# Kernel optimization log

Measured on AMD Instinct MI355X. Metric: run time of the kernel, lower is better.

The kernel has to match this reference:

```python
import jax, jax.numpy as jnp
import numpy as np

B, N, D, H = 4, 2048, 512, 8
KD = D // H  # per-head key/value dim = 64
NORM = 1.0 / np.sqrt(KD).astype(np.float32)


def setup_inputs() -> dict:
    key = jax.random.key(0)
    kq, km, k1, k2, k3 = jax.random.split(key, 5)
    s = 1.0 / np.sqrt(D)
    return {
        "queries": jax.random.normal(kq, (B, N, D), dtype=jnp.float32),
        "mask": jax.random.randint(km, (B, N, N), 0, 2).astype(jnp.bool_),
        "Wq": jax.random.normal(k1, (D, D), dtype=jnp.float32) * s,
        "Wk": jax.random.normal(k2, (D, D), dtype=jnp.float32) * s,
        "Wc": jax.random.normal(k3, (D, D), dtype=jnp.float32) * s,
    }


def reference(queries, mask, Wq, Wk, Wc):
    # Self-attention path (keys=None, values=None): V uses key_embed (Wk).
    Q = (queries @ Wq.T).reshape(B, N, H, KD)  # [B,N,H,kd]
    K = (queries @ Wk.T).reshape(B, N, H, KD)
    V = K  # original code: V = key_embed(queries) when values is None
    scores = NORM * jnp.einsum("bqhd,bkhd->bhqk", Q, K)  # [B,H,N,N]
    scores = jnp.where(mask[:, None, :, :], -jnp.inf, scores)
    attn = jax.nn.softmax(scores, axis=-1)
    out = jnp.einsum("bhqk,bkhd->bqhd", attn, V).reshape(B, N, H * KD)
    return out @ Wc.T  # [B,N,D]
```

## Files before the change

kernel.cpp:

```cpp
#include <hip/hip_runtime.h>
#include <hip/hip_bf16.h>
#include <math.h>

#define B_ 4
#define N_ 2048
#define D_ 512
#define H_ 8
#define NORM2_ 0.18033688011112042f

typedef __attribute__((ext_vector_type(8))) short short8;
typedef __attribute__((ext_vector_type(4))) float f32x4;
#define MFMA16(a, b, c) __builtin_amdgcn_mfma_f32_16x16x32_bf16(a, b, c, 0, 0, 0)
#define EXP2(x) __builtin_amdgcn_exp2f(x)

static __device__ __forceinline__ uint32_t pk2(float lo, float hi) {
  __hip_bfloat162 h = __float22bfloat162_rn(make_float2(lo, hi));
  return *(reinterpret_cast<uint32_t*>(&h));
}

static __device__ __forceinline__ void async16(const ushort* lds, const ushort* g) {
  __builtin_amdgcn_global_load_lds(
      (const __attribute__((address_space(1))) uint32_t*)g,
      (__attribute__((address_space(3))) uint32_t*)(ushort*)lds, 16, 0, 0);
}

__global__ __launch_bounds__(256) void prep(const float* __restrict__ q,
                                            const int* __restrict__ mask,
                                            const float* __restrict__ wq,
                                            const float* __restrict__ wk,
                                            const float* __restrict__ wc,
                                            ushort* __restrict__ Xb,
                                            ushort* __restrict__ Wb,
                                            uint32_t* __restrict__ pk) {
  const int bx = blockIdx.x;
  if (bx < 2048) {
    const int lane = threadIdx.x & 63;
    const int wid = ((bx << 8) + threadIdx.x) >> 6;
    for (int i = wid; i < 65536; i += 8192) {
      const int4 m = ((const int4*)mask)[(size_t)i * 64 + lane];
      uint32_t nib = (uint32_t)(m.x != 0) | ((uint32_t)(m.y != 0) << 1) |
                     ((uint32_t)(m.z != 0) << 2) | ((uint32_t)(m.w != 0) << 3);
      nib |= __shfl_xor(nib, 1) << 4;
      nib |= __shfl_xor(nib, 2) << 8;
      nib |= __shfl_xor(nib, 4) << 16;
      if ((lane & 7) == 0) pk[i * 8 + (lane >> 3)] = nib;
    }
  } else if (bx < 3072) {
    const int i = ((bx - 2048) << 8) + threadIdx.x;
    for (int j = i; j < 1048576; j += 262144) {
      const float4 v = ((const float4*)q)[j];
      uint2 o; o.x = pk2(v.x, v.y); o.y = pk2(v.z, v.w);
      ((uint2*)Xb)[j] = o;
    }
  } else {
    const int i = ((bx - 3072) << 8) + threadIdx.x;
    for (int j = i; j < 196608; j += 24576) {
      const int wi = j >> 16, off = j & 65535;
      const float* src = (wi == 0) ? wq : (wi == 1) ? wk : wc;
      const float4 v = ((const float4*)src)[off];
      uint2 o; o.x = pk2(v.x, v.y); o.y = pk2(v.z, v.w);
      ((uint2*)Wb)[j] = o;
    }
  }
}

template <int F32OUT>
__global__ __launch_bounds__(256) void gemm128(const ushort* __restrict__ X,
                                               const ushort* __restrict__ W0,
                                               const ushort* __restrict__ W1,
                                               void* __restrict__ C0,
                                               void* __restrict__ C1,
                                               float s0, float s1) {
  const ushort* Wp = (blockIdx.z == 0) ? W0 : W1;
  void* Cp = (blockIdx.z == 0) ? C0 : C1;
  const float sc = (blockIdx.z == 0) ? s0 : s1;
  const int t = threadIdx.x;
  const int w = t >> 6, lane = t & 63, quad = lane >> 4, c = lane & 15;
  const int wm = w & 1, wn = w >> 1;
  const int n0 = blockIdx.x * 128, m0 = blockIdx.y * 128;
  __shared__ __align__(16) ushort Xs[128][64];
  __shared__ __align__(16) ushort Ws[128][64];
  f32x4 acc[4][4];
#pragma unroll
  for (int i = 0; i < 4; ++i)
#pragma unroll
    for (int j = 0; j < 4; ++j) acc[i][j] = (f32x4){0.f, 0.f, 0.f, 0.f};

  for (int k0 = 0; k0 < D_; k0 += 64) {
    __syncthreads();
#pragma unroll
    for (int g = 0; g < 4; ++g) {
      const int id = w * 256 + g * 64 + lane;
      const int row = id >> 3, lch = id & 7;
      const int gch = lch ^ (row & 7);
      async16(&Xs[row][lch * 8], X + (size_t)(m0 + row) * D_ + k0 + gch * 8);
      async16(&Ws[row][lch * 8], Wp + (size_t)(n0 + row) * D_ + k0 + gch * 8);
    }
    __syncthreads();
#pragma unroll
    for (int s = 0; s < 2; ++s) {
      short8 af[4], bt[4];
#pragma unroll
      for (int i = 0; i < 4; ++i) {
        const int rA = wn * 64 + i * 16 + c;
        af[i] = *(const short8*)&Ws[rA][(((s * 4 + quad) ^ (rA & 7)) & 7) * 8];
        const int rB = wm * 64 + i * 16 + c;
        bt[i] = *(const short8*)&Xs[rB][(((s * 4 + quad) ^ (rB & 7)) & 7) * 8];
      }
#pragma unroll
      for (int i = 0; i < 4; ++i)
#pragma unroll
        for (int j = 0; j < 4; ++j) acc[i][j] = MFMA16(af[i], bt[j], acc[i][j]);
    }
  }
#pragma unroll
  for (int i = 0; i < 4; ++i)
#pragma unroll
    for (int j = 0; j < 4; ++j) {
      const size_t off =
          (size_t)(m0 + wm * 64 + j * 16 + c) * D_ + n0 + wn * 64 + i * 16 + quad * 4;
      if (F32OUT) {
        float4 v; v.x = acc[i][j][0]; v.y = acc[i][j][1]; v.z = acc[i][j][2]; v.w = acc[i][j][3];
        *(float4*)((float*)Cp + off) = v;
      } else {
        uint2 uv;
        uv.x = pk2(acc[i][j][0] * sc, acc[i][j][1] * sc);
        uv.y = pk2(acc[i][j][2] * sc, acc[i][j][3] * sc);
        *(uint2*)((ushort*)Cp + off) = uv;
      }
    }
}

__global__ __launch_bounds__(256) void attn_mfma(const ushort* __restrict__ Qb,
                                                 const ushort* __restrict__ Kb,
                                                 const uint32_t* __restrict__ pk,
                                                 ushort* __restrict__ Ab) {
  const int qt = blockIdx.x, h = blockIdx.y, b = blockIdx.z;
  const int q0 = qt * 64;
  const int t = threadIdx.x;
  const int w = t >> 6, lane = t & 63, quad = lane >> 4, c = lane & 15;

  __shared__ __align__(16) ushort Ks[64][64];
  __shared__ __align__(16) uint32_t KtU[64][32];
  __shared__ __align__(16) ushort QP[4][16][72];
  ushort(*Qs)[64] = (ushort(*)[64]) & QP[0][0][0];
  ushort(*Pq)[16][72] = QP;

#pragma unroll
  for (int p = 0; p < 2; ++p) {
    const int id = t + p * 256;
    const int row = id >> 3, lch = id & 7, gch = lch ^ (row & 7);
    async16(&Qs[row][lch * 8], Qb + (size_t)(b * N_ + q0 + row) * D_ + h * 64 + gch * 8);
  }
  __syncthreads();
  const int rq = (w << 4) + c;
  const short8 bq0 = *(const short8*)&Qs[rq][((quad ^ (rq & 7)) & 7) * 8];
  const short8 bq1 = *(const short8*)&Qs[rq][(((4 + quad) ^ (rq & 7)) & 7) * 8];

  short8 vones;
#pragma unroll
  for (int i = 0; i < 8; ++i) vones[i] = (short)0x3F80;

  f32x4 o[4];
#pragma unroll
  for (int i = 0; i < 4; ++i) o[i] = (f32x4){0.f, 0.f, 0.f, 0.f};
  f32x4 o5 = (f32x4){0.f, 0.f, 0.f, 0.f};

  const int kp = t >> 3, ch = t & 7;
  const int r0 = 2 * kp, r1 = r0 + 1;
  const int ksw0 = ((ch ^ (r0 & 7)) & 7) * 8, ksw1 = ((ch ^ (r1 & 7)) & 7) * 8;
  const ushort* kb0 = Kb + (size_t)(b * N_ + 2 * kp) * D_ + h * 64 + ch * 8;
  const uint32_t* pkq = pk + ((size_t)(b * N_ + q0 + (w << 4) + c) << 6);

  uint4 c0 = *(const uint4*)kb0;
  uint4 c1 = *(const uint4*)(kb0 + D_);
  uint2 cm = *(const uint2*)pkq;
  uint4 nx0, nx1; uint2 nxm;

  const int NT = N_ / 64;
  for (int kt = 0; kt < NT; ++kt) {
    __syncthreads();
    *(uint4*)&Ks[r0][ksw0] = c0;
    *(uint4*)&Ks[r1][ksw1] = c1;
    const uint32_t* a0 = (const uint32_t*)&c0;
    const uint32_t* a1 = (const uint32_t*)&c1;
#pragma unroll
    for (int m = 0; m < 4; ++m) {
      const uint32_t lo = __builtin_amdgcn_perm(a1[m], a0[m], 0x05040100);
      const uint32_t hi = __builtin_amdgcn_perm(a1[m], a0[m], 0x07060302);
      const int j0 = 2 * m, j1 = 2 * m + 1;
      KtU[ch * 8 + j0][(kp & 3) | ((((kp >> 2) ^ j0 ^ ch) & 7) << 2)] = lo;
      KtU[ch * 8 + j1][(kp & 3) | ((((kp >> 2) ^ j1 ^ ch) & 7) << 2)] = hi;
    }
    __syncthreads();

    if (kt + 1 < NT) {
      const ushort* kbn = kb0 + (size_t)(kt + 1) * 64 * D_;
      nx0 = *(const uint4*)kbn;
      nx1 = *(const uint4*)(kbn + D_);
      nxm = *(const uint2*)(pkq + (kt + 1) * 2);
    }

#pragma unroll
    for (int tI = 0; tI < 4; ++tI) {
      const int rk = tI * 16 + c;
      const short8 aK0 = *(const short8*)&Ks[rk][((quad ^ (rk & 7)) & 7) * 8];
      const short8 aK1 = *(const short8*)&Ks[rk][(((4 + quad) ^ (rk & 7)) & 7) * 8];
      f32x4 z = (f32x4){0.f, 0.f, 0.f, 0.f};
      z = MFMA16(aK0, bq0, z);
      z = MFMA16(aK1, bq1, z);
      const uint32_t mw = (tI < 2) ? cm.x : cm.y;
      const int bb = ((tI & 1) << 4) + quad * 4;
      uint32_t pb[4];
#pragma unroll
      for (int r = 0; r < 4; ++r) {
        const float e = EXP2(z[r]);
        pb[r] = ((mw >> (bb + r)) & 1u) ? 0u : __float_as_uint(e);
      }
      const uint32_t pw0 = __builtin_amdgcn_perm(pb[1], pb[0], 0x07060302);
      const uint32_t pw1 = __builtin_amdgcn_perm(pb[3], pb[2], 0x07060302);
      *(uint2*)&Pq[w][c][tI * 16 + quad * 4] = make_uint2(pw0, pw1);
    }

    const short8 bp0 = *(const short8*)&Pq[w][c][quad * 8];
    const short8 bp1 = *(const short8*)&Pq[w][c][32 + quad * 8];
    o5 = MFMA16(vones, bp0, o5);
    o5 = MFMA16(vones, bp1, o5);
#pragma unroll
    for (int dt = 0; dt < 4; ++dt) {
      const int dd = dt * 16 + c;
      const int g = (c & 7) ^ ((2 * dt + (c >> 3)) & 7);
      const short8 aV0 = *(const short8*)&KtU[dd][((quad ^ g) & 7) << 2];
      const short8 aV1 = *(const short8*)&KtU[dd][(((4 + quad) ^ g) & 7) << 2];
      o[dt] = MFMA16(aV0, bp0, o[dt]);
      o[dt] = MFMA16(aV1, bp1, o[dt]);
    }

    if (kt + 1 < NT) { c0 = nx0; c1 = nx1; cm = nxm; }
  }

  const float inv = 1.f / o5[0];
#pragma unroll
  for (int dt = 0; dt < 4; ++dt) {
    uint2 uv;
    uv.x = pk2(o[dt][0] * inv, o[dt][1] * inv);
    uv.y = pk2(o[dt][2] * inv, o[dt][3] * inv);
    *(uint2*)(Ab + (size_t)(b * N_ + q0 + (w << 4) + c) * D_ + h * 64 + dt * 16 + quad * 4) = uv;
  }
}

extern "C" void kernel_launch(void* const* d_in, const int* in_sizes, int n_in,
                              void* d_out, int out_size, void* d_ws, size_t ws_size,
                              hipStream_t stream) {
  const float* queries = (const float*)d_in[0];
  const int* mask = (const int*)d_in[1];
  const float* Wq = (const float*)d_in[2];
  const float* Wk = (const float*)d_in[3];
  const float* Wc = (const float*)d_in[4];
  float* out = (float*)d_out;

  const size_t nTok = (size_t)B_ * N_;
  const size_t nXD = nTok * D_;
  const size_t nW = (size_t)D_ * D_;
  ushort* Xb = (ushort*)d_ws;
  ushort* Wqb = Xb + nXD;
  ushort* Wkb = Wqb + nW;
  ushort* Wcb = Wkb + nW;
  ushort* Qb = Wcb + nW;
  ushort* Kb = Qb + nXD;
  ushort* Ab = Kb + nXD;
  uint32_t* pk = (uint32_t*)(Ab + nXD);

  prep<<<3168, 256, 0, stream>>>(queries, mask, Wq, Wk, Wc, Xb, Wqb, pk);
  gemm128<0><<<dim3(D_ / 128, (int)(nTok / 128), 2), 256, 0, stream>>>(
      Xb, Wqb, Wkb, Qb, Kb, NORM2_, 1.0f);
  attn_mfma<<<dim3(N_ / 64, H_, B_), 256, 0, stream>>>(Qb, Kb, pk, Ab);
  gemm128<1><<<dim3(D_ / 128, (int)(nTok / 128), 1), 256, 0, stream>>>(
      Ab, Wcb, nullptr, out, nullptr, 1.0f, 1.0f);
}
```

Baseline: 212.5 us.

## Split attention key tiles across waves and reduce partial outputs in LDS

Each wave now takes a 16-key slice of every 64-key tile for all 64 queries, where before each wave handled 16 queries over all keys. P stays in registers as the MFMA B operand with half-zero K padding, so the P round-trip through LDS and the ones-MFMA for the row sum both go away; the row sum is kept in scalar registers instead. Partial outputs from the four waves are combined afterwards through a rotating LDS reduction before normalisation. This trades more accumulator registers (16 f32x4) and half-empty MFMAs for removing per-tile LDS traffic and barriers around P.

```diff
diff --git a/kernel.cpp b/kernel.cpp
--- a/kernel.cpp
+++ b/kernel.cpp
@@ -10,6 +10,7 @@
 
 typedef __attribute__((ext_vector_type(8))) short short8;
 typedef __attribute__((ext_vector_type(4))) float f32x4;
+typedef __attribute__((ext_vector_type(2))) unsigned int u32x2;
 #define MFMA16(a, b, c) __builtin_amdgcn_mfma_f32_16x16x32_bf16(a, b, c, 0, 0, 0)
 #define EXP2(x) __builtin_amdgcn_exp2f(x)
 
@@ -135,16 +136,17 @@
                                                  const ushort* __restrict__ Kb,
                                                  const uint32_t* __restrict__ pk,
                                                  ushort* __restrict__ Ab) {
-  const int qt = blockIdx.x, h = blockIdx.y, b = blockIdx.z;
-  const int q0 = qt * 64;
+  const int qt64 = blockIdx.x, h = blockIdx.y, b = blockIdx.z;
+  const int q0 = qt64 * 64;
   const int t = threadIdx.x;
   const int w = t >> 6, lane = t & 63, quad = lane >> 4, c = lane & 15;
 
   __shared__ __align__(16) ushort Ks[64][64];
   __shared__ __align__(16) uint32_t KtU[64][32];
-  __shared__ __align__(16) ushort QP[4][16][72];
-  ushort(*Qs)[64] = (ushort(*)[64]) & QP[0][0][0];
-  ushort(*Pq)[16][72] = QP;
+  __shared__ __align__(16) unsigned char U[18432];
+  ushort(*Qs)[64] = (ushort(*)[64])U;
+  float* Ob = (float*)U;
+  float* lb = (float*)(U + 17408);
 
 #pragma unroll
   for (int p = 0; p < 2; ++p) {
@@ -152,30 +154,47 @@
     const int row = id >> 3, lch = id & 7, gch = lch ^ (row & 7);
     async16(&Qs[row][lch * 8], Qb + (size_t)(b * N_ + q0 + row) * D_ + h * 64 + gch * 8);
   }
-  __syncthreads();
-  const int rq = (w << 4) + c;
-  const short8 bq0 = *(const short8*)&Qs[rq][((quad ^ (rq & 7)) & 7) * 8];
-  const short8 bq1 = *(const short8*)&Qs[rq][(((4 + quad) ^ (rq & 7)) & 7) * 8];
-
-  short8 vones;
-#pragma unroll
-  for (int i = 0; i < 8; ++i) vones[i] = (short)0x3F80;
-
-  f32x4 o[4];
-#pragma unroll
-  for (int i = 0; i < 4; ++i) o[i] = (f32x4){0.f, 0.f, 0.f, 0.f};
-  f32x4 o5 = (f32x4){0.f, 0.f, 0.f, 0.f};
 
   const int kp = t >> 3, ch = t & 7;
   const int r0 = 2 * kp, r1 = r0 + 1;
   const int ksw0 = ((ch ^ (r0 & 7)) & 7) * 8, ksw1 = ((ch ^ (r1 & 7)) & 7) * 8;
   const ushort* kb0 = Kb + (size_t)(b * N_ + 2 * kp) * D_ + h * 64 + ch * 8;
-  const uint32_t* pkq = pk + ((size_t)(b * N_ + q0 + (w << 4) + c) << 6);
+  const uint32_t* mp = pk + ((size_t)(b * N_ + q0 + c) << 6) + (w >> 1);
 
   uint4 c0 = *(const uint4*)kb0;
   uint4 c1 = *(const uint4*)(kb0 + D_);
-  uint2 cm = *(const uint2*)pkq;
-  uint4 nx0, nx1; uint2 nxm;
+  uint32_t cm[4], nxm[4] = {0u, 0u, 0u, 0u};
+#pragma unroll
+  for (int qt = 0; qt < 4; ++qt) cm[qt] = mp[qt * 1024];
+  uint4 nx0, nx1;
+  __syncthreads();
+
+  short8 bq0[4], bq1[4];
+#pragma unroll
+  for (int qt = 0; qt < 4; ++qt) {
+    const int rq = qt * 16 + c;
+    bq0[qt] = *(const short8*)&Qs[rq][((quad ^ (rq & 7)) & 7) * 8];
+    bq1[qt] = *(const short8*)&Qs[rq][(((4 + quad) ^ (rq & 7)) & 7) * 8];
+  }
+
+  f32x4 o[4][4];
+#pragma unroll
+  for (int i = 0; i < 4; ++i)
+#pragma unroll
+    for (int j = 0; j < 4; ++j) o[i][j] = (f32x4){0.f, 0.f, 0.f, 0.f};
+  float l4[4] = {0.f, 0.f, 0.f, 0.f};
+
+  const int bb = (w & 1) * 16 + quad * 4;
+  const int rk = w * 16 + c;
+  const int akc0 = ((quad ^ (rk & 7)) & 7) * 8;
+  const int akc1 = (((4 + quad) ^ (rk & 7)) & 7) * 8;
+  const int p0lo = (2 * quad) & 3, p0hi = 2 * w + (quad >> 1);
+  int avcol[4];
+#pragma unroll
+  for (int dt = 0; dt < 4; ++dt) {
+    const int dd = dt * 16 + c;
+    avcol[dt] = dd * 32 + (p0lo | (((p0hi ^ (dd & 7) ^ (dd >> 3)) & 7) << 2));
+  }
 
   const int NT = N_ / 64;
   for (int kt = 0; kt < NT; ++kt) {
@@ -198,54 +217,94 @@
       const ushort* kbn = kb0 + (size_t)(kt + 1) * 64 * D_;
       nx0 = *(const uint4*)kbn;
       nx1 = *(const uint4*)(kbn + D_);
-      nxm = *(const uint2*)(pkq + (kt + 1) * 2);
-    }
-
-#pragma unroll
-    for (int tI = 0; tI < 4; ++tI) {
-      const int rk = tI * 16 + c;
-      const short8 aK0 = *(const short8*)&Ks[rk][((quad ^ (rk & 7)) & 7) * 8];
-      const short8 aK1 = *(const short8*)&Ks[rk][(((4 + quad) ^ (rk & 7)) & 7) * 8];
-      f32x4 z = (f32x4){0.f, 0.f, 0.f, 0.f};
-      z = MFMA16(aK0, bq0, z);
-      z = MFMA16(aK1, bq1, z);
-      const uint32_t mw = (tI < 2) ? cm.x : cm.y;
-      const int bb = ((tI & 1) << 4) + quad * 4;
-      uint32_t pb[4];
+#pragma unroll
+      for (int qt = 0; qt < 4; ++qt) nxm[qt] = mp[qt * 1024 + (kt + 1) * 2];
+    }
+
+    const short8 aK0 = *(const short8*)&Ks[rk][akc0];
+    const short8 aK1 = *(const short8*)&Ks[rk][akc1];
+    f32x4 z[4];
+#pragma unroll
+    for (int qt = 0; qt < 4; ++qt) {
+      f32x4 zz = (f32x4){0.f, 0.f, 0.f, 0.f};
+      zz = MFMA16(aK0, bq0[qt], zz);
+      zz = MFMA16(aK1, bq1[qt], zz);
+      z[qt] = zz;
+    }
+    short8 av8[4];
+#pragma unroll
+    for (int dt = 0; dt < 4; ++dt) {
+      const u32x2 vv = *(const u32x2*)&((const uint32_t*)KtU)[avcol[dt]];
+      const uint4 va = make_uint4(vv[0], vv[1], 0u, 0u);
+      av8[dt] = __builtin_bit_cast(short8, va);
+    }
+    short8 pb8[4];
+#pragma unroll
+    for (int qt = 0; qt < 4; ++qt) {
+      const uint32_t mw = cm[qt];
+      float pf[4];
 #pragma unroll
       for (int r = 0; r < 4; ++r) {
-        const float e = EXP2(z[r]);
-        pb[r] = ((mw >> (bb + r)) & 1u) ? 0u : __float_as_uint(e);
+        const float e = EXP2(z[qt][r]);
+        pf[r] = ((mw >> (bb + r)) & 1u) ? 0.f : e;
       }
-      const uint32_t pw0 = __builtin_amdgcn_perm(pb[1], pb[0], 0x07060302);
-      const uint32_t pw1 = __builtin_amdgcn_perm(pb[3], pb[2], 0x07060302);
-      *(uint2*)&Pq[w][c][tI * 16 + quad * 4] = make_uint2(pw0, pw1);
-    }
-
-    const short8 bp0 = *(const short8*)&Pq[w][c][quad * 8];
-    const short8 bp1 = *(const short8*)&Pq[w][c][32 + quad * 8];
-    o5 = MFMA16(vones, bp0, o5);
-    o5 = MFMA16(vones, bp1, o5);
+      l4[qt] += (pf[0] + pf[1]) + (pf[2] + pf[3]);
+      const uint4 uu = make_uint4(pk2(pf[0], pf[1]), pk2(pf[2], pf[3]), 0u, 0u);
+      pb8[qt] = __builtin_bit_cast(short8, uu);
+      cm[qt] = nxm[qt];
+    }
+#pragma unroll
+    for (int dt = 0; dt < 4; ++dt)
+#pragma unroll
+      for (int qt = 0; qt < 4; ++qt) o[dt][qt] = MFMA16(av8[dt], pb8[qt], o[dt][qt]);
+
+    c0 = nx0; c1 = nx1;
+  }
+
+#pragma unroll
+  for (int qt = 0; qt < 4; ++qt) {
+    l4[qt] += __shfl_xor(l4[qt], 16);
+    l4[qt] += __shfl_xor(l4[qt], 32);
+  }
+  const float lv = (quad == 0) ? l4[0] : (quad == 1) ? l4[1] : (quad == 2) ? l4[2] : l4[3];
+  lb[w * 64 + quad * 16 + c] = lv;
+
+#pragma unroll
+  for (int s = 0; s < 4; ++s) {
+    if (s) __syncthreads();
+    const int mydt = (w + s) & 3;
 #pragma unroll
     for (int dt = 0; dt < 4; ++dt) {
-      const int dd = dt * 16 + c;
-      const int g = (c & 7) ^ ((2 * dt + (c >> 3)) & 7);
-      const short8 aV0 = *(const short8*)&KtU[dd][((quad ^ g) & 7) << 2];
-      const short8 aV1 = *(const short8*)&KtU[dd][(((4 + quad) ^ g) & 7) << 2];
-      o[dt] = MFMA16(aV0, bp0, o[dt]);
-      o[dt] = MFMA16(aV1, bp1, o[dt]);
-    }
-
-    if (kt + 1 < NT) { c0 = nx0; c1 = nx1; cm = nxm; }
-  }
-
-  const float inv = 1.f / o5[0];
+      if (dt != mydt) continue;
+#pragma unroll
+      for (int qt = 0; qt < 4; ++qt)
+#pragma unroll
+        for (int jj = 0; jj < 4; ++jj) {
+          float* p = &Ob[(dt * 16 + quad * 4 + jj) * 68 + qt * 16 + c];
+          if (s == 0) *p = o[dt][qt][jj];
+          else if (s < 3) *p += o[dt][qt][jj];
+          else o[dt][qt][jj] += *p;
+        }
+    }
+  }
+
+  float inv[4];
+#pragma unroll
+  for (int qt = 0; qt < 4; ++qt)
+    inv[qt] = 1.f / (lb[qt * 16 + c] + lb[64 + qt * 16 + c] + lb[128 + qt * 16 + c] +
+                     lb[192 + qt * 16 + c]);
+  const int dqf = (w + 3) & 3;
 #pragma unroll
   for (int dt = 0; dt < 4; ++dt) {
-    uint2 uv;
-    uv.x = pk2(o[dt][0] * inv, o[dt][1] * inv);
-    uv.y = pk2(o[dt][2] * inv, o[dt][3] * inv);
-    *(uint2*)(Ab + (size_t)(b * N_ + q0 + (w << 4) + c) * D_ + h * 64 + dt * 16 + quad * 4) = uv;
+    if (dt != dqf) continue;
+#pragma unroll
+    for (int qt = 0; qt < 4; ++qt) {
+      uint2 uv;
+      uv.x = pk2(o[dt][qt][0] * inv[qt], o[dt][qt][1] * inv[qt]);
+      uv.y = pk2(o[dt][qt][2] * inv[qt], o[dt][qt][3] * inv[qt]);
+      *(uint2*)(Ab + (size_t)(b * N_ + q0 + qt * 16 + c) * D_ + h * 64 + dt * 16 +
+                quad * 4) = uv;
+    }
   }
 }
 
```

New measurement: 242.8 us. +14.3%, slower.

## Use byte mask with AND-masking, XCD-aware block remap, and MFMA priority

Applied to the files above, without the earlier changes.

The mask is now expanded in prep to one byte per element (0xFF keep, 0 masked) instead of bit-packed words. The attention kernel builds masks with byte permutes and ANDs the packed bf16 probabilities, which removes per-element shift-and-select. Blocks use a 1D grid remapped so that blocks sharing (b, head) land on the same XCD for K reuse in L2, and s_setprio raises priority around the PV MFMA section. In exchange, the mask buffer is 8x larger, adding write traffic in prep and read traffic in attention.

```diff
diff --git a/kernel.cpp b/kernel.cpp
--- a/kernel.cpp
+++ b/kernel.cpp
@@ -31,19 +31,15 @@
                                             const float* __restrict__ wc,
                                             ushort* __restrict__ Xb,
                                             ushort* __restrict__ Wb,
-                                            uint32_t* __restrict__ pk) {
+                                            uint32_t* __restrict__ mb) {
   const int bx = blockIdx.x;
   if (bx < 2048) {
-    const int lane = threadIdx.x & 63;
-    const int wid = ((bx << 8) + threadIdx.x) >> 6;
-    for (int i = wid; i < 65536; i += 8192) {
-      const int4 m = ((const int4*)mask)[(size_t)i * 64 + lane];
-      uint32_t nib = (uint32_t)(m.x != 0) | ((uint32_t)(m.y != 0) << 1) |
-                     ((uint32_t)(m.z != 0) << 2) | ((uint32_t)(m.w != 0) << 3);
-      nib |= __shfl_xor(nib, 1) << 4;
-      nib |= __shfl_xor(nib, 2) << 8;
-      nib |= __shfl_xor(nib, 4) << 16;
-      if ((lane & 7) == 0) pk[i * 8 + (lane >> 3)] = nib;
+    const int gid = (bx << 8) + threadIdx.x;
+    for (int i = gid; i < 4194304; i += 524288) {
+      const int4 m = ((const int4*)mask)[i];
+      const uint32_t v = (m.x ? 0u : 0xFFu) | (m.y ? 0u : 0xFF00u) |
+                         (m.z ? 0u : 0xFF0000u) | (m.w ? 0u : 0xFF000000u);
+      mb[i] = v;
     }
   } else if (bx < 3072) {
     const int i = ((bx - 2048) << 8) + threadIdx.x;
@@ -133,10 +129,12 @@
 
 __global__ __launch_bounds__(256) void attn_mfma(const ushort* __restrict__ Qb,
                                                  const ushort* __restrict__ Kb,
-                                                 const uint32_t* __restrict__ pk,
+                                                 const unsigned char* __restrict__ mb,
                                                  ushort* __restrict__ Ab) {
-  const int qt = blockIdx.x, h = blockIdx.y, b = blockIdx.z;
-  const int q0 = qt * 64;
+  const int Lx = blockIdx.x;
+  const int wk = ((Lx & 7) << 7) | (Lx >> 3);
+  const int h = wk & 7, qt64 = (wk >> 3) & 31, b = wk >> 8;
+  const int q0 = qt64 * 64;
   const int t = threadIdx.x;
   const int w = t >> 6, lane = t & 63, quad = lane >> 4, c = lane & 15;
 
@@ -170,12 +168,15 @@
   const int r0 = 2 * kp, r1 = r0 + 1;
   const int ksw0 = ((ch ^ (r0 & 7)) & 7) * 8, ksw1 = ((ch ^ (r1 & 7)) & 7) * 8;
   const ushort* kb0 = Kb + (size_t)(b * N_ + 2 * kp) * D_ + h * 64 + ch * 8;
-  const uint32_t* pkq = pk + ((size_t)(b * N_ + q0 + (w << 4) + c) << 6);
+  const uint32_t* mrow =
+      (const uint32_t*)(mb + (size_t)(b * N_ + q0 + (w << 4) + c) * N_) + quad;
 
   uint4 c0 = *(const uint4*)kb0;
   uint4 c1 = *(const uint4*)(kb0 + D_);
-  uint2 cm = *(const uint2*)pkq;
-  uint4 nx0, nx1; uint2 nxm;
+  uint32_t cm[4], nxm[4];
+#pragma unroll
+  for (int tI = 0; tI < 4; ++tI) cm[tI] = mrow[(tI & 1) * 4 + (tI >> 1) * 8];
+  uint4 nx0, nx1;
 
   const int NT = N_ / 64;
   for (int kt = 0; kt < NT; ++kt) {
@@ -198,7 +199,9 @@
       const ushort* kbn = kb0 + (size_t)(kt + 1) * 64 * D_;
       nx0 = *(const uint4*)kbn;
       nx1 = *(const uint4*)(kbn + D_);
-      nxm = *(const uint2*)(pkq + (kt + 1) * 2);
+#pragma unroll
+      for (int tI = 0; tI < 4; ++tI)
+        nxm[tI] = mrow[(kt + 1) * 16 + (tI & 1) * 4 + (tI >> 1) * 8];
     }
 
 #pragma unroll
@@ -209,21 +212,20 @@
       f32x4 z = (f32x4){0.f, 0.f, 0.f, 0.f};
       z = MFMA16(aK0, bq0, z);
       z = MFMA16(aK1, bq1, z);
-      const uint32_t mw = (tI < 2) ? cm.x : cm.y;
-      const int bb = ((tI & 1) << 4) + quad * 4;
+      const uint32_t mw = cm[tI];
+      const uint32_t mlo = __builtin_amdgcn_perm(mw, mw, 0x01010000);
+      const uint32_t mhi = __builtin_amdgcn_perm(mw, mw, 0x03030202);
       uint32_t pb[4];
 #pragma unroll
-      for (int r = 0; r < 4; ++r) {
-        const float e = EXP2(z[r]);
-        pb[r] = ((mw >> (bb + r)) & 1u) ? 0u : __float_as_uint(e);
-      }
-      const uint32_t pw0 = __builtin_amdgcn_perm(pb[1], pb[0], 0x07060302);
-      const uint32_t pw1 = __builtin_amdgcn_perm(pb[3], pb[2], 0x07060302);
+      for (int r = 0; r < 4; ++r) pb[r] = __float_as_uint(EXP2(z[r]));
+      const uint32_t pw0 = __builtin_amdgcn_perm(pb[1], pb[0], 0x07060302) & mlo;
+      const uint32_t pw1 = __builtin_amdgcn_perm(pb[3], pb[2], 0x07060302) & mhi;
       *(uint2*)&Pq[w][c][tI * 16 + quad * 4] = make_uint2(pw0, pw1);
     }
 
     const short8 bp0 = *(const short8*)&Pq[w][c][quad * 8];
     const short8 bp1 = *(const short8*)&Pq[w][c][32 + quad * 8];
+    __builtin_amdgcn_s_setprio(1);
     o5 = MFMA16(vones, bp0, o5);
     o5 = MFMA16(vones, bp1, o5);
 #pragma unroll
@@ -235,8 +237,13 @@
       o[dt] = MFMA16(aV0, bp0, o[dt]);
       o[dt] = MFMA16(aV1, bp1, o[dt]);
     }
-
-    if (kt + 1 < NT) { c0 = nx0; c1 = nx1; cm = nxm; }
+    __builtin_amdgcn_s_setprio(0);
+
+    if (kt + 1 < NT) {
+      c0 = nx0; c1 = nx1;
+#pragma unroll
+      for (int tI = 0; tI < 4; ++tI) cm[tI] = nxm[tI];
+    }
   }
 
   const float inv = 1.f / o5[0];
@@ -269,12 +276,13 @@
   ushort* Qb = Wcb + nW;
   ushort* Kb = Qb + nXD;
   ushort* Ab = Kb + nXD;
-  uint32_t* pk = (uint32_t*)(Ab + nXD);
-
-  prep<<<3168, 256, 0, stream>>>(queries, mask, Wq, Wk, Wc, Xb, Wqb, pk);
+  uint32_t* mb = (uint32_t*)(Ab + nXD);
+
+  prep<<<3168, 256, 0, stream>>>(queries, mask, Wq, Wk, Wc, Xb, Wqb, mb);
   gemm128<0><<<dim3(D_ / 128, (int)(nTok / 128), 2), 256, 0, stream>>>(
       Xb, Wqb, Wkb, Qb, Kb, NORM2_, 1.0f);
-  attn_mfma<<<dim3(N_ / 64, H_, B_), 256, 0, stream>>>(Qb, Kb, pk, Ab);
+  attn_mfma<<<dim3(N_ / 64 * H_ * B_), 256, 0, stream>>>(
+      Qb, Kb, (const unsigned char*)mb, Ab);
   gemm128<1><<<dim3(D_ / 128, (int)(nTok / 128), 1), 256, 0, stream>>>(
       Ab, Wcb, nullptr, out, nullptr, 1.0f, 1.0f);
 }
```

New measurement: 224.4 us. 5.6% more time.

## Split attention key range in two and merge partial outputs in a new kernel

Applied to the files above, without the earlier changes.

The attention kernel now splits the 2048 keys into two halves, one per block, which doubles the grid so each block runs 16 key tiles instead of 32. Each half writes an unnormalized bf16 partial output and its softmax denominator into reused workspace (Xb, Ab, Wqb, Wkb). A new elementwise merge kernel adds the two partials and divides by the summed denominators before the output projection. The aim is more parallel blocks and shorter per-block runtime. In exchange it adds a kernel launch, extra global traffic, a duplicated Q load per block, and bf16 rounding of the unnormalized partial sums.

```diff
diff --git a/kernel.cpp b/kernel.cpp
--- a/kernel.cpp
+++ b/kernel.cpp
@@ -64,6 +64,32 @@
   }
 }
 
+__global__ __launch_bounds__(256) void merge(const ushort* __restrict__ P0,
+                                             const float* __restrict__ l0,
+                                             const float* __restrict__ l1,
+                                             ushort* __restrict__ Ab) {
+  const int j = (blockIdx.x << 8) + threadIdx.x;
+  const int h = (j >> 3) & 7;
+  const int tok = j >> 6;
+  const int b = tok >> 11, n = tok & 2047;
+  const int li = ((b * H_ + h) << 11) + n;
+  const float inv = 1.f / (l0[li] + l1[li]);
+  const uint4 a0 = ((const uint4*)P0)[j];
+  const uint4 a1 = ((const uint4*)Ab)[j];
+  uint4 o;
+  const uint32_t* u0 = (const uint32_t*)&a0;
+  const uint32_t* u1 = (const uint32_t*)&a1;
+  uint32_t* uo = (uint32_t*)&o;
+#pragma unroll
+  for (int m = 0; m < 4; ++m) {
+    const float lo = __uint_as_float(u0[m] << 16) + __uint_as_float(u1[m] << 16);
+    const float hi = __uint_as_float(u0[m] & 0xFFFF0000u) +
+                     __uint_as_float(u1[m] & 0xFFFF0000u);
+    uo[m] = pk2(lo * inv, hi * inv);
+  }
+  ((uint4*)Ab)[j] = o;
+}
+
 template <int F32OUT>
 __global__ __launch_bounds__(256) void gemm128(const ushort* __restrict__ X,
                                                const ushort* __restrict__ W0,
@@ -134,9 +160,13 @@
 __global__ __launch_bounds__(256) void attn_mfma(const ushort* __restrict__ Qb,
                                                  const ushort* __restrict__ Kb,
                                                  const uint32_t* __restrict__ pk,
-                                                 ushort* __restrict__ Ab) {
-  const int qt = blockIdx.x, h = blockIdx.y, b = blockIdx.z;
-  const int q0 = qt * 64;
+                                                 ushort* __restrict__ P0,
+                                                 ushort* __restrict__ P1,
+                                                 float* __restrict__ l0,
+                                                 float* __restrict__ l1) {
+  const int qt64 = blockIdx.x >> 1, hf = blockIdx.x & 1;
+  const int h = blockIdx.y, b = blockIdx.z;
+  const int q0 = qt64 * 64;
   const int t = threadIdx.x;
   const int w = t >> 6, lane = t & 63, quad = lane >> 4, c = lane & 15;
 
@@ -169,15 +199,17 @@
   const int kp = t >> 3, ch = t & 7;
   const int r0 = 2 * kp, r1 = r0 + 1;
   const int ksw0 = ((ch ^ (r0 & 7)) & 7) * 8, ksw1 = ((ch ^ (r1 & 7)) & 7) * 8;
-  const ushort* kb0 = Kb + (size_t)(b * N_ + 2 * kp) * D_ + h * 64 + ch * 8;
-  const uint32_t* pkq = pk + ((size_t)(b * N_ + q0 + (w << 4) + c) << 6);
+  const ushort* kb0 =
+      Kb + (size_t)(b * N_ + hf * 1024 + 2 * kp) * D_ + h * 64 + ch * 8;
+  const uint32_t* pkq =
+      pk + ((size_t)(b * N_ + q0 + (w << 4) + c) << 6) + hf * 32;
 
   uint4 c0 = *(const uint4*)kb0;
   uint4 c1 = *(const uint4*)(kb0 + D_);
   uint2 cm = *(const uint2*)pkq;
   uint4 nx0, nx1; uint2 nxm;
 
-  const int NT = N_ / 64;
+  const int NT = 16;
   for (int kt = 0; kt < NT; ++kt) {
     __syncthreads();
     *(uint4*)&Ks[r0][ksw0] = c0;
@@ -239,14 +271,16 @@
     if (kt + 1 < NT) { c0 = nx0; c1 = nx1; cm = nxm; }
   }
 
-  const float inv = 1.f / o5[0];
+  ushort* Pp = hf ? P1 : P0;
+  float* lp = hf ? l1 : l0;
 #pragma unroll
   for (int dt = 0; dt < 4; ++dt) {
     uint2 uv;
-    uv.x = pk2(o[dt][0] * inv, o[dt][1] * inv);
-    uv.y = pk2(o[dt][2] * inv, o[dt][3] * inv);
-    *(uint2*)(Ab + (size_t)(b * N_ + q0 + (w << 4) + c) * D_ + h * 64 + dt * 16 + quad * 4) = uv;
-  }
+    uv.x = pk2(o[dt][0], o[dt][1]);
+    uv.y = pk2(o[dt][2], o[dt][3]);
+    *(uint2*)(Pp + (size_t)(b * N_ + q0 + (w << 4) + c) * D_ + h * 64 + dt * 16 + quad * 4) = uv;
+  }
+  if (quad == 0) lp[((b * H_ + h) << 11) + q0 + (w << 4) + c] = o5[0];
 }
 
 extern "C" void kernel_launch(void* const* d_in, const int* in_sizes, int n_in,
@@ -270,11 +304,16 @@
   ushort* Kb = Qb + nXD;
   ushort* Ab = Kb + nXD;
   uint32_t* pk = (uint32_t*)(Ab + nXD);
+  ushort* P0 = Xb;
+  ushort* P1 = Ab;
+  float* l0 = (float*)Wqb;
+  float* l1 = (float*)Wkb;
 
   prep<<<3168, 256, 0, stream>>>(queries, mask, Wq, Wk, Wc, Xb, Wqb, pk);
   gemm128<0><<<dim3(D_ / 128, (int)(nTok / 128), 2), 256, 0, stream>>>(
       Xb, Wqb, Wkb, Qb, Kb, NORM2_, 1.0f);
-  attn_mfma<<<dim3(N_ / 64, H_, B_), 256, 0, stream>>>(Qb, Kb, pk, Ab);
+  attn_mfma<<<dim3(64, H_, B_), 256, 0, stream>>>(Qb, Kb, pk, P0, P1, l0, l1);
+  merge<<<2048, 256, 0, stream>>>(P0, l0, l1, Ab);
   gemm128<1><<<dim3(D_ / 128, (int)(nTok / 128), 1), 256, 0, stream>>>(
       Ab, Wcb, nullptr, out, nullptr, 1.0f, 1.0f);
 }
```

Result: no change. 214.7 us (+1.0%).
